# Performance work log

Measured on AMD Instinct MI355X. Metric: run time of the kernel, lower is better.

Reference implementation:

```python
import jax, jax.numpy as jnp
import numpy as np

B, C, H, W = 8, 64, 128, 128
K = 3            # deformable kernel size
DIL = 1          # dilation == padding for the deformable conv
OFF_K = 2 * (DIL + 1) + 1   # = 5, offset-conv kernel
OFF_PAD = DIL + 1            # = 2, same-padding for offset conv
KK = K * K


def setup_inputs() -> dict:
    key = jax.random.key(0)
    k1, k2, k3, k4 = jax.random.split(key, 4)
    x = jax.random.normal(k1, (B, C, H, W), dtype=jnp.float32)
    weights = jax.random.normal(k2, (C, C, K, K), dtype=jnp.float32) * 0.05
    offset_w = jax.random.normal(k3, (2 * KK, C, OFF_K, OFF_K), dtype=jnp.float32) * 0.02
    offset_b = jax.random.normal(k4, (2 * KK,), dtype=jnp.float32) * 0.01
    return {"x": x, "weights": weights, "offset_w": offset_w, "offset_b": offset_b}


def _deform_conv2d(x, weights, off):
    # x: [B,C,H,W]; weights: [O,C,K,K]; off: [B,2*KK,H,W] (dy,dx interleaved per tap)
    b, c, h, w = x.shape
    o = weights.shape[0]
    off = off.reshape(b, KK, 2, h, w)
    dy = off[:, :, 0]            # [B,KK,H,W]
    dx = off[:, :, 1]
    ti = jnp.arange(KK) // K     # kernel row per tap
    tj = jnp.arange(KK) % K      # kernel col per tap
    ygrid = jnp.arange(h, dtype=jnp.float32)
    xgrid = jnp.arange(w, dtype=jnp.float32)
    # sample position: out_pos - pad + tap*dilation + offset
    base_y = (ti * DIL - DIL).astype(jnp.float32)  # pad = DIL
    base_x = (tj * DIL - DIL).astype(jnp.float32)
    py = ygrid[None, None, :, None] + base_y[None, :, None, None] + dy  # [B,KK,H,W]
    px = xgrid[None, None, None, :] + base_x[None, :, None, None] + dx

    def sample_one(img, py_b, px_b):
        # img: [C,H,W]; py_b/px_b: [KK,H,W] -> [C,KK,H,W]
        y0 = jnp.floor(py_b)
        x0 = jnp.floor(px_b)
        fy = py_b - y0
        fx = px_b - x0
        y0i = y0.astype(jnp.int32)
        x0i = x0.astype(jnp.int32)

        def corner(yi, xi, wgt):
            valid = (yi >= 0) & (yi < h) & (xi >= 0) & (xi < w)
            v = img[:, jnp.clip(yi, 0, h - 1), jnp.clip(xi, 0, w - 1)]  # [C,KK,H,W]
            return v * (wgt * valid)[None]

        return (corner(y0i, x0i, (1 - fy) * (1 - fx))
                + corner(y0i, x0i + 1, (1 - fy) * fx)
                + corner(y0i + 1, x0i, fy * (1 - fx))
                + corner(y0i + 1, x0i + 1, fy * fx))

    sampled = jax.vmap(sample_one)(x, py, px)            # [B,C,KK,H,W]
    return jnp.einsum('bctyx,oct->boyx', sampled, weights.reshape(o, c, KK))


def reference(x, weights, offset_w, offset_b):
    # offset conv (same padding) + Hardtanh clamp to [-1,1]
    off = jax.lax.conv_general_dilated(
        x, offset_w, window_strides=(1, 1),
        padding=[(OFF_PAD, OFF_PAD), (OFF_PAD, OFF_PAD)],
        dimension_numbers=('NCHW', 'OIHW', 'NCHW'))
    off = off + offset_b[None, :, None, None]
    off = jnp.clip(off, -1.0, 1.0)
    return _deform_conv2d(x, weights, off)
```

## Files before the change

### kernel.cpp

```cpp
#include <hip/hip_runtime.h>

#define BB  8
#define CC  64
#define HH  128
#define WW  128
#define OCC 18
#define XP  133
#define SP  72
#define XTP 68

typedef __attribute__((ext_vector_type(8)))  short bf16x8;
typedef __attribute__((ext_vector_type(16))) float f32x16;

static __device__ __forceinline__ ushort f2bf(float f) {
    union { float f; unsigned u; } v; v.f = f;
    unsigned r = (v.u + 0x7FFFu + ((v.u >> 16) & 1u)) >> 16;
    return (ushort)r;
}
static __device__ __forceinline__ float bfu(unsigned u) {
    union { unsigned u; float f; } v; v.u = u; return v.f;
}

__global__ __launch_bounds__(256) void prep_kernel(
    const float* __restrict__ x, const float* __restrict__ w,
    const float* __restrict__ ow, ushort* __restrict__ XT,
    ushort* __restrict__ WAf, ushort* __restrict__ WDf)
{
    __shared__ ushort T[64 * XTP];
    const int tid = threadIdx.x;
    const int phys = blockIdx.x;

    if (phys >= 2 * BB * HH) {
        int id = phys - 2 * BB * HH;
        if (id < 200) {
            int idx = id * 256 + tid;
            int j  = idx & 7;
            int l  = (idx >> 3) & 63;
            int cs = (idx >> 9) & 3;
            int t  = idx >> 11;
            int oc = l & 31;
            int c  = cs * 16 + (l >> 5) * 8 + j;
            float v = (oc < OCC) ? ow[((size_t)(oc * CC + c)) * 25 + t] : 0.f;
            WAf[idx] = f2bf(v);
        } else {
            int idx = (id - 200) * 256 + tid;
            int j  = idx & 7;
            int l  = (idx >> 3) & 63;
            int cs = (idx >> 9) & 3;
            int mt = (idx >> 11) & 1;
            int t  = idx >> 12;
            int o  = mt * 32 + (l & 31);
            int c  = cs * 16 + (l >> 5) * 8 + j;
            WDf[idx] = f2bf(w[((size_t)(o * CC + c)) * 9 + t]);
        }
        return;
    }

    const int b    = phys & 7;
    const int idx  = phys >> 3;
    const int half = idx & 1;
    const int y    = idx >> 1;

    {
        int j = idx * 256 + tid;
        if (j < 5 * XP * 8) {
            int r   = j / (XP * 8);
            int off = j % (XP * 8);
            int yp  = (r < 2) ? r : (128 + r);
            ((uint4*)(XT + ((size_t)b * XP + yp) * XP * 64))[off] = make_uint4(0, 0, 0, 0);
        }
    }

    {
        const int pg = tid & 15;
        const int p0 = pg * 4;
        const int c0 = tid >> 4;
        const float* xb = x + (size_t)b * CC * HH * WW + (size_t)y * WW + half * 64;
#pragma unroll
        for (int i = 0; i < 4; i++) {
            int c = c0 + 16 * i;
            float4 v = *(const float4*)&xb[(size_t)c * HH * WW + p0];
            T[(p0 + 0) * XTP + c] = f2bf(v.x);
            T[(p0 + 1) * XTP + c] = f2bf(v.y);
            T[(p0 + 2) * XTP + c] = f2bf(v.z);
            T[(p0 + 3) * XTP + c] = f2bf(v.w);
        }
    }
    __syncthreads();

    ushort* orow = XT + (((size_t)b * XP + (y + 2)) * XP) * 64;

    if (half == 0) {
        if (tid < 16) {
            int col = tid >> 3;
            ((uint4*)(orow + (size_t)col * 64))[tid & 7] = make_uint4(0, 0, 0, 0);
        }
    } else {
        if (tid < 24) {
            int col = 130 + (tid >> 3);
            ((uint4*)(orow + (size_t)col * 64))[tid & 7] = make_uint4(0, 0, 0, 0);
        }
    }

#pragma unroll
    for (int g = 0; g < 2; g++) {
        int i2 = g * 256 + tid;
        int pl = i2 >> 3;
        int part = i2 & 7;
        uint2 lo = *(const uint2*)&T[pl * XTP + part * 8];
        uint2 hi = *(const uint2*)&T[pl * XTP + part * 8 + 4];
        uint4 wv; wv.x = lo.x; wv.y = lo.y; wv.z = hi.x; wv.w = hi.y;
        ((uint4*)(orow + ((size_t)(half * 64 + pl + 2)) * 64))[part] = wv;
    }
}

__global__ __launch_bounds__(256, 6) void fused_kernel(
    const ushort* __restrict__ XT, const ushort* __restrict__ WAf,
    const ushort* __restrict__ WDf, const float* __restrict__ ob,
    float* __restrict__ out)
{
    __shared__ __align__(16) char smem[68 * SP * 2];
    __shared__ float off_lds[OCC * 64];

    const int tid   = threadIdx.x;
    const int lane  = tid & 63;
    const int n     = lane & 31;
    const int h     = lane >> 5;
    const int w     = tid >> 6;
    const int ptile = w & 1;
    const int tset  = w >> 1;

    const int b    = blockIdx.x & 7;
    const int idx  = blockIdx.x >> 3;
    const int half = idx & 1;
    const int y    = idx >> 1;

    {
        ushort* XROW = (ushort*)smem;
        float*  red  = (float*)smem;
        f32x16 acc = {};
        const ushort* src0 = XT + (((size_t)b * XP + y) * XP + half * 64) * 64;

        for (int ky = 0; ky < 5; ky++) {
            if (ky) __syncthreads();
            const ushort* src = src0 + (size_t)ky * XP * 64;
            for (int i = tid; i < 68 * 8; i += 256) {
                int pl = i >> 3, ch = (i & 7) * 8;
                *(uint4*)&XROW[pl * SP + ch] = *(const uint4*)(src + (size_t)pl * 64 + ch);
            }
            __syncthreads();

#pragma unroll
            for (int kx = 0; kx < 5; kx++) {
                const int t = ky * 5 + kx;
                const ushort* bbase = &XROW[(ptile * 32 + n + kx) * SP + h * 8];
#pragma unroll
                for (int c2 = 0; c2 < 2; c2++) {
                    const int cs = tset * 2 + c2;
                    bf16x8 af = *(const bf16x8*)(WAf + (((size_t)t * 4 + cs) * 64 + lane) * 8);
                    bf16x8 bf = *(const bf16x8*)(bbase + cs * 16);
                    acc = __builtin_amdgcn_mfma_f32_32x32x16_bf16(af, bf, acc, 0, 0, 0);
                }
            }
        }
        __syncthreads();
        if (tset == 1) {
#pragma unroll
            for (int r = 0; r < 16; r++)
                red[ptile * 1024 + r * 64 + lane] = acc[r];
        }
        __syncthreads();
        if (tset == 0) {
#pragma unroll
            for (int r = 0; r < 16; r++) {
                int oc = (r & 3) + 8 * (r >> 2) + 4 * h;
                if (oc < OCC) {
                    float v = acc[r] + red[ptile * 1024 + r * 64 + lane] + ob[oc];
                    v = fminf(fmaxf(v, -1.f), 1.f);
                    off_lds[oc * 64 + ptile * 32 + n] = v;
                }
            }
        }
        __syncthreads();
    }

    ushort* S = (ushort*)smem;
    const int p   = tid >> 2;
    const int cs4 = (tid & 3) * 16;

    const int m0 = ptile * 32;
    const int n0 = tset * 32;

    f32x16 acc = {};
    const ushort* xtb = XT + (size_t)b * XP * XP * 64;

    for (int t = 0; t < 9; t++) {
        float dy = off_lds[(2 * t) * 64 + p];
        float dx = off_lds[(2 * t + 1) * 64 + p];
        float py = (float)(y + t / 3 - 1) + dy;
        float px = (float)(half * 64 + p + t % 3 - 1) + dx;
        float y0f = floorf(py), x0f = floorf(px);
        float fy = py - y0f, fx = px - x0f;
        int iy = (int)y0f + 2, ix = (int)x0f + 2;
        float w00 = (1.f - fy) * (1.f - fx), w01 = (1.f - fy) * fx;
        float w10 = fy * (1.f - fx),         w11 = fy * fx;

        const ushort* c00 = xtb + ((size_t)iy * XP + ix) * 64 + cs4;
        const ushort* c10 = c00 + XP * 64;

        uint4 q[8];
        q[0] = *(const uint4*)(c00);      q[1] = *(const uint4*)(c00 + 8);
        q[2] = *(const uint4*)(c00 + 64); q[3] = *(const uint4*)(c00 + 72);
        q[4] = *(const uint4*)(c10);      q[5] = *(const uint4*)(c10 + 8);
        q[6] = *(const uint4*)(c10 + 64); q[7] = *(const uint4*)(c10 + 72);

        __syncthreads();

#pragma unroll
        for (int m = 0; m < 2; m++) {
            unsigned o4[4];
#pragma unroll
            for (int j = 0; j < 4; j++) {
                unsigned u00 = ((const unsigned*)&q[m])[j];
                unsigned u01 = ((const unsigned*)&q[2 + m])[j];
                unsigned u10 = ((const unsigned*)&q[4 + m])[j];
                unsigned u11 = ((const unsigned*)&q[6 + m])[j];
                float lo = w00 * bfu(u00 << 16) + w01 * bfu(u01 << 16)
                         + w10 * bfu(u10 << 16) + w11 * bfu(u11 << 16);
                float hi = w00 * bfu(u00 & 0xffff0000u) + w01 * bfu(u01 & 0xffff0000u)
                         + w10 * bfu(u10 & 0xffff0000u) + w11 * bfu(u11 & 0xffff0000u);
                o4[j] = (unsigned)f2bf(lo) | ((unsigned)f2bf(hi) << 16);
            }
            *(uint4*)&S[p * SP + cs4 + m * 8] = *(uint4*)o4;
        }
        __syncthreads();

        const ushort* bp = &S[(n0 + n) * SP + h * 8];
#pragma unroll
        for (int cs = 0; cs < 4; cs++) {
            bf16x8 af = *(const bf16x8*)(WDf + ((((size_t)t * 2 + ptile) * 4 + cs) * 64 + lane) * 8);
            bf16x8 bf = *(const bf16x8*)(bp + cs * 16);
            acc = __builtin_amdgcn_mfma_f32_32x32x16_bf16(af, bf, acc, 0, 0, 0);
        }
    }

#pragma unroll
    for (int r = 0; r < 16; r++) {
        int o = m0 + (r & 3) + 8 * (r >> 2) + 4 * h;
        out[((size_t)(b * CC + o) * HH + y) * WW + half * 64 + n0 + n] = acc[r];
    }
}

extern "C" void kernel_launch(void* const* d_in, const int* in_sizes, int n_in,
                              void* d_out, int out_size, void* d_ws, size_t ws_size,
                              hipStream_t stream)
{
    const float* x  = (const float*)d_in[0];
    const float* w  = (const float*)d_in[1];
    const float* ow = (const float*)d_in[2];
    const float* ob = (const float*)d_in[3];
    float* out = (float*)d_out;

    ushort* XT  = (ushort*)d_ws;
    ushort* WAf = (ushort*)((char*)d_ws + 18113536);
    ushort* WDf = (ushort*)((char*)d_ws + 18215936);

    prep_kernel<<<2 * BB * HH + 344, 256, 0, stream>>>(x, w, ow, XT, WAf, WDf);
    fused_kernel<<<2 * BB * HH, 256, 0, stream>>>(XT, WAf, WDf, ob, out);
}
```

Before: 148.7 us.

## Apply bilinear weights after MFMA per corner instead of interpolating before

Instead of blending the four bilinear corners in fp32 on VALU and storing one interpolated tile, each corner's raw bf16 samples are written to a separate LDS tile. Four MFMA chains run, one per corner, and each partial result is scaled by that corner's per-pixel weight before being accumulated. This removes the per-element unpack, interpolate and round work but quadruples MFMA count and LDS footprint. The occupancy bound drops from 6 to 3 blocks.

```diff
diff --git a/kernel.cpp b/kernel.cpp
--- a/kernel.cpp
+++ b/kernel.cpp
@@ -114,13 +114,14 @@
     }
 }
 
-__global__ __launch_bounds__(256, 6) void fused_kernel(
+__global__ __launch_bounds__(256, 3) void fused_kernel(
     const ushort* __restrict__ XT, const ushort* __restrict__ WAf,
     const ushort* __restrict__ WDf, const float* __restrict__ ob,
     float* __restrict__ out)
 {
-    __shared__ __align__(16) char smem[68 * SP * 2];
+    __shared__ __align__(16) char smem[4 * 64 * SP * 2];
     __shared__ float off_lds[OCC * 64];
+    __shared__ float wlds[4 * 64];
 
     const int tid   = threadIdx.x;
     const int lane  = tid & 63;
@@ -186,12 +187,14 @@
 
     ushort* S = (ushort*)smem;
     const int p   = tid >> 2;
-    const int cs4 = (tid & 3) * 16;
+    const int jj  = tid & 3;
+    const int cs4 = jj * 16;
 
     const int m0 = ptile * 32;
     const int n0 = tset * 32;
 
     f32x16 acc = {};
+    f32x16 kZero = {};
     const ushort* xtb = XT + (size_t)b * XP * XP * 64;
 
     for (int t = 0; t < 9; t++) {
@@ -204,6 +207,7 @@
         int iy = (int)y0f + 2, ix = (int)x0f + 2;
         float w00 = (1.f - fy) * (1.f - fx), w01 = (1.f - fy) * fx;
         float w10 = fy * (1.f - fx),         w11 = fy * fx;
+        float wj = (jj == 0) ? w00 : (jj == 1) ? w01 : (jj == 2) ? w10 : w11;
 
         const ushort* c00 = xtb + ((size_t)iy * XP + ix) * 64 + cs4;
         const ushort* c10 = c00 + XP * 64;
@@ -217,30 +221,28 @@
         __syncthreads();
 
 #pragma unroll
-        for (int m = 0; m < 2; m++) {
-            unsigned o4[4];
-#pragma unroll
-            for (int j = 0; j < 4; j++) {
-                unsigned u00 = ((const unsigned*)&q[m])[j];
-                unsigned u01 = ((const unsigned*)&q[2 + m])[j];
-                unsigned u10 = ((const unsigned*)&q[4 + m])[j];
-                unsigned u11 = ((const unsigned*)&q[6 + m])[j];
-                float lo = w00 * bfu(u00 << 16) + w01 * bfu(u01 << 16)
-                         + w10 * bfu(u10 << 16) + w11 * bfu(u11 << 16);
-                float hi = w00 * bfu(u00 & 0xffff0000u) + w01 * bfu(u01 & 0xffff0000u)
-                         + w10 * bfu(u10 & 0xffff0000u) + w11 * bfu(u11 & 0xffff0000u);
-                o4[j] = (unsigned)f2bf(lo) | ((unsigned)f2bf(hi) << 16);
-            }
-            *(uint4*)&S[p * SP + cs4 + m * 8] = *(uint4*)o4;
-        }
-        __syncthreads();
-
-        const ushort* bp = &S[(n0 + n) * SP + h * 8];
-#pragma unroll
-        for (int cs = 0; cs < 4; cs++) {
-            bf16x8 af = *(const bf16x8*)(WDf + ((((size_t)t * 2 + ptile) * 4 + cs) * 64 + lane) * 8);
-            bf16x8 bf = *(const bf16x8*)(bp + cs * 16);
-            acc = __builtin_amdgcn_mfma_f32_32x32x16_bf16(af, bf, acc, 0, 0, 0);
+        for (int k = 0; k < 4; k++) {
+            *(uint4*)&S[(size_t)k * 64 * SP + p * SP + cs4]     = q[2 * k];
+            *(uint4*)&S[(size_t)k * 64 * SP + p * SP + cs4 + 8] = q[2 * k + 1];
+        }
+        wlds[jj * 64 + p] = wj;
+        __syncthreads();
+
+        bf16x8 af[4];
+#pragma unroll
+        for (int cs = 0; cs < 4; cs++)
+            af[cs] = *(const bf16x8*)(WDf + ((((size_t)t * 2 + ptile) * 4 + cs) * 64 + lane) * 8);
+
+#pragma unroll
+        for (int k = 0; k < 4; k++) {
+            const ushort* bp = &S[(size_t)k * 64 * SP + (n0 + n) * SP + h * 8];
+            f32x16 pk = __builtin_amdgcn_mfma_f32_32x32x16_bf16(af[0], *(const bf16x8*)(bp), kZero, 0, 0, 0);
+            pk = __builtin_amdgcn_mfma_f32_32x32x16_bf16(af[1], *(const bf16x8*)(bp + 16), pk, 0, 0, 0);
+            pk = __builtin_amdgcn_mfma_f32_32x32x16_bf16(af[2], *(const bf16x8*)(bp + 32), pk, 0, 0, 0);
+            pk = __builtin_amdgcn_mfma_f32_32x32x16_bf16(af[3], *(const bf16x8*)(bp + 48), pk, 0, 0, 0);
+            float wk = wlds[k * 64 + n0 + n];
+#pragma unroll
+            for (int r = 0; r < 16; r++) acc[r] += wk * pk[r];
         }
     }
 
```

Result: slower. 287.7 us (+93.5%).
